# Kernel optimization log

Measured on AMD Instinct MI355X. Metric: run time of the kernel, lower is better.

## Reference

```python
import jax, jax.numpy as jnp
import numpy as np

N_SRC = 100000
N_DST = 50000
N_EDGES = 1600000
D_IN = 128
D_OUT = 64


def setup_inputs() -> dict:
    key = jax.random.key(0)
    ks = jax.random.split(key, 6)
    x = jax.random.normal(ks[0], (N_SRC, D_IN), dtype=jnp.float32)
    W_l = jax.random.normal(ks[1], (D_IN, D_OUT), dtype=jnp.float32) * (1.0 / np.sqrt(D_IN))
    b_l = jax.random.normal(ks[2], (D_OUT,), dtype=jnp.float32) * 0.01
    W_r = jax.random.normal(ks[3], (D_IN, D_OUT), dtype=jnp.float32) * (1.0 / np.sqrt(D_IN))
    src = jax.random.randint(ks[4], (N_EDGES,), 0, N_SRC, dtype=jnp.int64)
    dst = jax.random.randint(ks[5], (N_EDGES,), 0, N_DST, dtype=jnp.int64)
    edge_index = jnp.stack([src, dst], axis=0)
    return {"x": x, "W_l": W_l, "b_l": b_l, "W_r": W_r,
            "edge_index": edge_index, "n_dst": N_DST}


def reference(x, W_l, b_l, W_r, edge_index, n_dst):
    src, dst = edge_index[0], edge_index[1]
    # gather source features along edges: [E, D_in]
    msgs = x[src]
    # mean aggregation at destination nodes
    agg = jax.ops.segment_sum(msgs, dst, num_segments=n_dst)          # [n_dst, D_in]
    cnt = jax.ops.segment_sum(jnp.ones_like(dst, dtype=x.dtype), dst,
                              num_segments=n_dst)                     # [n_dst]
    mean = agg / jnp.maximum(cnt, 1.0)[:, None]
    x_target = x[:n_dst]
    # SAGEConv: lin_l(mean_agg) + lin_r(x_target)
    out = mean @ W_l + b_l + x_target @ W_r                           # [n_dst, D_out]
    return jax.nn.log_softmax(out, axis=-1)
```

## Files before the change

### kernel.cpp

```cpp
#include <hip/hip_runtime.h>
#include <math.h>

#define DIN  128
#define DOUT 64
#define PROWS 64
#define KS   32
#define XSP  36
#define BSH  6
#define BMSK 63
#define BCAP 2496

__device__ inline unsigned short f2bf(float f) {
    unsigned u = __float_as_uint(f);
    u += 0x7fffu + ((u >> 16) & 1u);
    return (unsigned short)(u >> 16);
}
__device__ inline float bflo(unsigned u) { return __uint_as_float(u << 16); }
__device__ inline float bfhi(unsigned u) { return __uint_as_float(u & 0xffff0000u); }

__global__ void __launch_bounds__(256) build_k(
    const int* __restrict__ ei, unsigned* __restrict__ gTail,
    int* __restrict__ bucketBuf,
    const float* __restrict__ x, const float* __restrict__ Wl,
    const float* __restrict__ bl, const float* __restrict__ Wr,
    unsigned short* __restrict__ y, float* __restrict__ zout,
    int E, int nFill, int P, int nyb, int n_src, int n_dst, int nB)
{
    __shared__ float s_mem[PROWS * XSP + KS * DOUT];
    const int b = blockIdx.x;
    const int fq = b / P;
    const bool isFill = ((b % P) == 0) && (fq < nFill);

    if (isFill) {
        int* s_i  = (int*)s_mem;
        int* lcnt = s_i;
        int* lpos = s_i + 1024;
        int* s_gb = s_i + 2048;
        const int t = threadIdx.x;
        const int myb = (fq * 256 + t) * 8;
        const bool full = (myb + 8 <= E);
        const bool any  = (myb < E);
        int4 sa, sb4, da, db;
        if (full) {
            sa  = *(const int4*)(ei + myb);
            sb4 = *(const int4*)(ei + myb + 4);
            da  = *(const int4*)(ei + E + myb);
            db  = *(const int4*)(ei + E + myb + 4);
        }
        lcnt[t] = 0; lcnt[t + 256] = 0; lcnt[t + 512] = 0; lcnt[t + 768] = 0;
        lpos[t] = 0; lpos[t + 256] = 0; lpos[t + 512] = 0; lpos[t + 768] = 0;
        __syncthreads();
        if (full) {
            atomicAdd(&lcnt[da.x >> BSH], 1); atomicAdd(&lcnt[da.y >> BSH], 1);
            atomicAdd(&lcnt[da.z >> BSH], 1); atomicAdd(&lcnt[da.w >> BSH], 1);
            atomicAdd(&lcnt[db.x >> BSH], 1); atomicAdd(&lcnt[db.y >> BSH], 1);
            atomicAdd(&lcnt[db.z >> BSH], 1); atomicAdd(&lcnt[db.w >> BSH], 1);
        } else if (any) {
            for (int i = myb; i < E && i < myb + 8; ++i)
                atomicAdd(&lcnt[ei[E + i] >> BSH], 1);
        }
        __syncthreads();
        for (int bk = t; bk < nB; bk += 256)
            s_gb[bk] = (int)atomicAdd(&gTail[bk], (unsigned)lcnt[bk]);
        __syncthreads();
#define PLACE(S, D) { int bk = (D) >> BSH; int p = atomicAdd(&lpos[bk], 1);          \
                      unsigned pos = (unsigned)(s_gb[bk] + p);                        \
                      if (pos < BCAP) bucketBuf[(size_t)bk * BCAP + pos] =            \
                          ((S) << BSH) | ((D) & BMSK); }
        if (full) {
            PLACE(sa.x,  da.x) PLACE(sa.y,  da.y) PLACE(sa.z,  da.z) PLACE(sa.w,  da.w)
            PLACE(sb4.x, db.x) PLACE(sb4.y, db.y) PLACE(sb4.z, db.z) PLACE(sb4.w, db.w)
        } else if (any) {
            for (int i = myb; i < E && i < myb + 8; ++i) {
                int s = ei[i], d = ei[E + i];
                PLACE(s, d)
            }
        }
#undef PLACE
        return;
    }

    const int fillsBefore = (fq + 1 < nFill) ? (fq + 1) : nFill;
    const int pb = b - fillsBefore;
    const int t  = threadIdx.x;
    const bool isY = (pb < nyb);
    const int rowBase = (isY ? pb : pb - nyb) * PROWS;
    const int nRows = isY ? n_src : n_dst;
    const float* __restrict__ W = isY ? Wl : Wr;

    float* s_xs = s_mem;
    float* s_ws = s_mem + PROWS * XSP;

    const int cg = t & 15;
    const int rg = t >> 4;
    const int r0 = rg * 4;

    float4 acc0 = {0.f,0.f,0.f,0.f};
    float4 acc1 = {0.f,0.f,0.f,0.f};
    float4 acc2 = {0.f,0.f,0.f,0.f};
    float4 acc3 = {0.f,0.f,0.f,0.f};

#define ROWFMA(acc, xv)                                                                     \
    acc.x = fmaf(xv.w, w3.x, fmaf(xv.z, w2.x, fmaf(xv.y, w1.x, fmaf(xv.x, w0.x, acc.x)))); \
    acc.y = fmaf(xv.w, w3.y, fmaf(xv.z, w2.y, fmaf(xv.y, w1.y, fmaf(xv.x, w0.y, acc.y)))); \
    acc.z = fmaf(xv.w, w3.z, fmaf(xv.z, w2.z, fmaf(xv.y, w1.z, fmaf(xv.x, w0.z, acc.z)))); \
    acc.w = fmaf(xv.w, w3.w, fmaf(xv.z, w2.w, fmaf(xv.y, w1.w, fmaf(xv.x, w0.w, acc.w))));

    for (int k0 = 0; k0 < DIN; k0 += KS) {
        {
            const float* xs = x + (size_t)rowBase * DIN + k0;
            #pragma unroll
            for (int j = 0; j < 2; ++j) {
                int fi = t + 256 * j;
                int row = fi >> 3, c4 = fi & 7;
                if (rowBase + row < nRows) {
                    float4 v = *(const float4*)(xs + (size_t)row * DIN + c4 * 4);
                    *(float4*)(&s_xs[row * XSP + c4 * 4]) = v;
                }
            }
            const float* ws = W + (size_t)k0 * DOUT;
            #pragma unroll
            for (int j = 0; j < 2; ++j) {
                int fi = t + 256 * j;
                int row = fi >> 4, c4 = fi & 15;
                float4 v = *(const float4*)(ws + row * DOUT + c4 * 4);
                *(float4*)(&s_ws[row * DOUT + c4 * 4]) = v;
            }
        }
        __syncthreads();

        const float* wp = s_ws + cg * 4;
        #pragma unroll 2
        for (int k = 0; k < KS; k += 4) {
            float4 w0 = *(const float4*)(wp + (k + 0) * DOUT);
            float4 w1 = *(const float4*)(wp + (k + 1) * DOUT);
            float4 w2 = *(const float4*)(wp + (k + 2) * DOUT);
            float4 w3 = *(const float4*)(wp + (k + 3) * DOUT);
            float4 x0 = *(const float4*)(&s_xs[(r0 + 0) * XSP + k]);
            float4 x1 = *(const float4*)(&s_xs[(r0 + 1) * XSP + k]);
            float4 x2 = *(const float4*)(&s_xs[(r0 + 2) * XSP + k]);
            float4 x3 = *(const float4*)(&s_xs[(r0 + 3) * XSP + k]);
            ROWFMA(acc0, x0)
            ROWFMA(acc1, x1)
            ROWFMA(acc2, x2)
            ROWFMA(acc3, x3)
        }
        __syncthreads();
    }
#undef ROWFMA

    if (isY) {
        float4 av[4] = {acc0, acc1, acc2, acc3};
        #pragma unroll
        for (int r = 0; r < 4; ++r) {
            int row = rowBase + r0 + r;
            if (row < nRows) {
                uint2 pk;
                pk.x = (unsigned)f2bf(av[r].x) | ((unsigned)f2bf(av[r].y) << 16);
                pk.y = (unsigned)f2bf(av[r].z) | ((unsigned)f2bf(av[r].w) << 16);
                *(uint2*)(y + (size_t)row * DOUT + cg * 4) = pk;
            }
        }
    } else {
        const float4 bv = *(const float4*)(bl + cg * 4);
        float4 av[4] = {acc0, acc1, acc2, acc3};
        #pragma unroll
        for (int r = 0; r < 4; ++r) {
            int row = rowBase + r0 + r;
            if (row < nRows) {
                float4 o;
                o.x = av[r].x + bv.x; o.y = av[r].y + bv.y;
                o.z = av[r].z + bv.z; o.w = av[r].w + bv.w;
                *(float4*)(zout + (size_t)row * DOUT + cg * 4) = o;
            }
        }
    }
}

__global__ void __launch_bounds__(512) bg_k(
    const unsigned* __restrict__ gTail, const int* __restrict__ bucketBuf,
    const unsigned short* __restrict__ y,
    float* __restrict__ out, int n_dst)
{
    __shared__ int s_ent[BCAP];
    __shared__ int s_csr[BCAP];
    __shared__ int s_hist[64];
    __shared__ int s_ofs[64];
    __shared__ int s_start[65];
    const int b = blockIdx.x, t = threadIdx.x;
    const int lane = t & 63, wave = t >> 6;

    if (t < 64) s_hist[t] = 0;
    int m = (int)gTail[b]; if (m > BCAP) m = BCAP;
    __syncthreads();

    const int* bb = bucketBuf + (size_t)b * BCAP;
    const int4* bb4 = (const int4*)bb;
    int4* se4 = (int4*)s_ent;
    const int m4 = m >> 2;
    for (int i4 = t; i4 < m4; i4 += 512) {
        int4 e4 = bb4[i4];
        se4[i4] = e4;
        atomicAdd(&s_hist[e4.x & BMSK], 1);
        atomicAdd(&s_hist[e4.y & BMSK], 1);
        atomicAdd(&s_hist[e4.z & BMSK], 1);
        atomicAdd(&s_hist[e4.w & BMSK], 1);
    }
    for (int i = (m4 << 2) + t; i < m; i += 512) {
        int e = bb[i];
        s_ent[i] = e;
        atomicAdd(&s_hist[e & BMSK], 1);
    }
    __syncthreads();

    if (wave == 0) {
        int h = s_hist[lane];
        int v = h;
        for (int o = 1; o < 64; o <<= 1) {
            int u = __shfl_up(v, o);
            if (lane >= o) v += u;
        }
        s_start[lane + 1] = v;
        if (lane == 0) s_start[0] = 0;
        s_ofs[lane] = v - h;
    }
    __syncthreads();

    for (int i4 = t; i4 < m4; i4 += 512) {
        int4 e4 = se4[i4];
        int p0 = atomicAdd(&s_ofs[e4.x & BMSK], 1); s_csr[p0] = e4.x >> BSH;
        int p1 = atomicAdd(&s_ofs[e4.y & BMSK], 1); s_csr[p1] = e4.y >> BSH;
        int p2 = atomicAdd(&s_ofs[e4.z & BMSK], 1); s_csr[p2] = e4.z >> BSH;
        int p3 = atomicAdd(&s_ofs[e4.w & BMSK], 1); s_csr[p3] = e4.w >> BSH;
    }
    for (int i = (m4 << 2) + t; i < m; i += 512) {
        int e = s_ent[i];
        int p = atomicAdd(&s_ofs[e & BMSK], 1);
        s_csr[p] = e >> BSH;
    }
    __syncthreads();

    const int dbase = b << BSH;
    int nloc = n_dst - dbase; if (nloc > 64) nloc = 64;
    const int g  = lane >> 3;
    const int c8 = lane & 7;
    const uint4* yw = (const uint4*)y;

#define ACC8(al, ah, u)                                              \
    al.x += bflo(u.x); al.y += bfhi(u.x);                            \
    al.z += bflo(u.y); al.w += bfhi(u.y);                            \
    ah.x += bflo(u.z); ah.y += bfhi(u.z);                            \
    ah.z += bflo(u.w); ah.w += bfhi(u.w);

    for (int r = wave; r < nloc; r += 8) {
        const int row = dbase + r;
        const int start = s_start[r];
        const int deg = s_start[r + 1] - start;

        const float4 zv0 = *(const float4*)(out + (size_t)row * DOUT + c8 * 8);
        const float4 zv1 = *(const float4*)(out + (size_t)row * DOUT + c8 * 8 + 4);

        float4 a0l = {0,0,0,0}, a0h = {0,0,0,0};
        float4 a1l = {0,0,0,0}, a1h = {0,0,0,0};
        float4 a2l = {0,0,0,0}, a2h = {0,0,0,0};
        float4 a3l = {0,0,0,0}, a3h = {0,0,0,0};

        for (int co = 0; co < deg; co += 64) {
            int rem = deg - co; if (rem > 64) rem = 64;
            int idx = (lane < rem) ? s_csr[start + co + lane] : 0;
            int i = 0;
            for (; i + 32 <= rem; i += 32) {
                int s0 = __shfl(idx, i + g);
                int s1 = __shfl(idx, i + 8 + g);
                int s2 = __shfl(idx, i + 16 + g);
                int s3 = __shfl(idx, i + 24 + g);
                uint4 u0 = yw[(size_t)s0 * 8 + c8];
                uint4 u1 = yw[(size_t)s1 * 8 + c8];
                uint4 u2 = yw[(size_t)s2 * 8 + c8];
                uint4 u3 = yw[(size_t)s3 * 8 + c8];
                ACC8(a0l, a0h, u0)
                ACC8(a1l, a1h, u1)
                ACC8(a2l, a2h, u2)
                ACC8(a3l, a3h, u3)
            }
            for (; i < rem; i += 8) {
                int e = i + g;
                int s0 = __shfl(idx, e);
                if (e < rem) {
                    uint4 u = yw[(size_t)s0 * 8 + c8];
                    ACC8(a0l, a0h, u)
                }
            }
        }

        float4 sl, sh;
        sl.x = (a0l.x + a1l.x) + (a2l.x + a3l.x);
        sl.y = (a0l.y + a1l.y) + (a2l.y + a3l.y);
        sl.z = (a0l.z + a1l.z) + (a2l.z + a3l.z);
        sl.w = (a0l.w + a1l.w) + (a2l.w + a3l.w);
        sh.x = (a0h.x + a1h.x) + (a2h.x + a3h.x);
        sh.y = (a0h.y + a1h.y) + (a2h.y + a3h.y);
        sh.z = (a0h.z + a1h.z) + (a2h.z + a3h.z);
        sh.w = (a0h.w + a1h.w) + (a2h.w + a3h.w);

        #pragma unroll
        for (int o = 32; o >= 8; o >>= 1) {
            sl.x += __shfl_xor(sl.x, o); sl.y += __shfl_xor(sl.y, o);
            sl.z += __shfl_xor(sl.z, o); sl.w += __shfl_xor(sl.w, o);
            sh.x += __shfl_xor(sh.x, o); sh.y += __shfl_xor(sh.y, o);
            sh.z += __shfl_xor(sh.z, o); sh.w += __shfl_xor(sh.w, o);
        }

        const float scale = 1.0f / (float)(deg > 0 ? deg : 1);
        float4 v0, v1;
        v0.x = sl.x * scale + zv0.x; v0.y = sl.y * scale + zv0.y;
        v0.z = sl.z * scale + zv0.z; v0.w = sl.w * scale + zv0.w;
        v1.x = sh.x * scale + zv1.x; v1.y = sh.y * scale + zv1.y;
        v1.z = sh.z * scale + zv1.z; v1.w = sh.w * scale + zv1.w;

        float mx = fmaxf(fmaxf(fmaxf(v0.x, v0.y), fmaxf(v0.z, v0.w)),
                         fmaxf(fmaxf(v1.x, v1.y), fmaxf(v1.z, v1.w)));
        for (int o = 4; o >= 1; o >>= 1) mx = fmaxf(mx, __shfl_xor(mx, o));
        float s = expf(v0.x - mx) + expf(v0.y - mx) + expf(v0.z - mx) + expf(v0.w - mx)
                + expf(v1.x - mx) + expf(v1.y - mx) + expf(v1.z - mx) + expf(v1.w - mx);
        for (int o = 4; o >= 1; o >>= 1) s += __shfl_xor(s, o);
        const float lse = mx + logf(s);

        if (lane < 8) {
            float4 o0, o1;
            o0.x = v0.x - lse; o0.y = v0.y - lse; o0.z = v0.z - lse; o0.w = v0.w - lse;
            o1.x = v1.x - lse; o1.y = v1.y - lse; o1.z = v1.z - lse; o1.w = v1.w - lse;
            *(float4*)(out + (size_t)row * DOUT + c8 * 8)     = o0;
            *(float4*)(out + (size_t)row * DOUT + c8 * 8 + 4) = o1;
        }
    }
#undef ACC8
}

extern "C" void kernel_launch(void* const* d_in, const int* in_sizes, int n_in,
                              void* d_out, int out_size, void* d_ws, size_t ws_size,
                              hipStream_t stream)
{
    const float* x  = (const float*)d_in[0];
    const float* Wl = (const float*)d_in[1];
    const float* bl = (const float*)d_in[2];
    const float* Wr = (const float*)d_in[3];
    const int*   ei = (const int*)d_in[4];

    const int E     = in_sizes[4] / 2;
    const int n_src = in_sizes[0] / DIN;
    const int n_dst = out_size / DOUT;
    const int nB    = (n_dst + (1 << BSH) - 1) >> BSH;

    unsigned* gTail = (unsigned*)d_ws;
    int* bucketBuf = (int*)d_ws + 1024;
    unsigned short* yb = (unsigned short*)(bucketBuf + (size_t)nB * BCAP);

    hipMemsetAsync(gTail, 0, 1024 * sizeof(unsigned), stream);

    int nFill = (E + 2047) / 2048;
    int nyb = (n_src + PROWS - 1) / PROWS;
    int nzb = (n_dst + PROWS - 1) / PROWS;
    int total = nFill + nyb + nzb;
    int P = (total + nFill - 1) / nFill;

    build_k<<<total, 256, 0, stream>>>(
        ei, gTail, bucketBuf, x, Wl, bl, Wr, yb, (float*)d_out,
        E, nFill, P, nyb, n_src, n_dst, nB);

    bg_k<<<nB, 512, 0, stream>>>(gTail, bucketBuf, yb, (float*)d_out, n_dst);
}
```

Before: 200.5 us.

## Use direct global-to-LDS loads with XOR swizzle and pad bucket tail counters

The projection tiles now load straight into LDS through the global_load_lds builtin instead of staging through registers. The padded x tile is replaced by an XOR-swizzled layout so the reads stay free of bank conflicts. Bucket tail counters are spread GSTR words apart to cut atomic contention and false sharing across cache lines, which makes the memset larger. The direct LDS load has alignment and layout rules on AMD hardware, and tail rows with no loaded data now leave stale LDS contents.

Result: slower. 215.1 us (+7.3%).

```diff
diff --git a/kernel.cpp b/kernel.cpp
--- a/kernel.cpp
+++ b/kernel.cpp
@@ -5,10 +5,10 @@
 #define DOUT 64
 #define PROWS 64
 #define KS   32
-#define XSP  36
 #define BSH  6
 #define BMSK 63
 #define BCAP 2496
+#define GSTR 16
 
 __device__ inline unsigned short f2bf(float f) {
     unsigned u = __float_as_uint(f);
@@ -17,6 +17,12 @@
 }
 __device__ inline float bflo(unsigned u) { return __uint_as_float(u << 16); }
 __device__ inline float bfhi(unsigned u) { return __uint_as_float(u & 0xffff0000u); }
+
+__device__ inline void gl16(const float* g, float* l) {
+    __builtin_amdgcn_global_load_lds(
+        (const __attribute__((address_space(1))) unsigned int*)g,
+        (__attribute__((address_space(3))) unsigned int*)l, 16, 0, 0);
+}
 
 __global__ void __launch_bounds__(256) build_k(
     const int* __restrict__ ei, unsigned* __restrict__ gTail,
@@ -26,7 +32,7 @@
     unsigned short* __restrict__ y, float* __restrict__ zout,
     int E, int nFill, int P, int nyb, int n_src, int n_dst, int nB)
 {
-    __shared__ float s_mem[PROWS * XSP + KS * DOUT];
+    __shared__ float s_mem[4096];
     const int b = blockIdx.x;
     const int fq = b / P;
     const bool isFill = ((b % P) == 0) && (fq < nFill);
@@ -61,7 +67,7 @@
         }
         __syncthreads();
         for (int bk = t; bk < nB; bk += 256)
-            s_gb[bk] = (int)atomicAdd(&gTail[bk], (unsigned)lcnt[bk]);
+            s_gb[bk] = (int)atomicAdd(&gTail[(size_t)bk * GSTR], (unsigned)lcnt[bk]);
         __syncthreads();
 #define PLACE(S, D) { int bk = (D) >> BSH; int p = atomicAdd(&lpos[bk], 1);          \
                       unsigned pos = (unsigned)(s_gb[bk] + p);                        \
@@ -89,11 +95,21 @@
     const float* __restrict__ W = isY ? Wl : Wr;
 
     float* s_xs = s_mem;
-    float* s_ws = s_mem + PROWS * XSP;
+    float* s_ws = s_mem + 2048;
 
     const int cg = t & 15;
     const int rg = t >> 4;
     const int r0 = rg * 4;
+
+    const int xrow0 = t >> 3,        xc0 = t & 7;
+    const int xrow1 = (t + 256) >> 3, xc1 = (t + 256) & 7;
+    const int xs0 = (xc0 ^ (xrow0 & 7)) * 4;
+    const int xs1 = (xc1 ^ (xrow1 & 7)) * 4;
+
+    const int xb0 = (r0 + 0) * 32, xm0 = (r0 + 0) & 7;
+    const int xb1 = (r0 + 1) * 32, xm1 = (r0 + 1) & 7;
+    const int xb2 = (r0 + 2) * 32, xm2 = (r0 + 2) & 7;
+    const int xb3 = (r0 + 3) * 32, xm3 = (r0 + 3) & 7;
 
     float4 acc0 = {0.f,0.f,0.f,0.f};
     float4 acc1 = {0.f,0.f,0.f,0.f};
@@ -109,37 +125,28 @@
     for (int k0 = 0; k0 < DIN; k0 += KS) {
         {
             const float* xs = x + (size_t)rowBase * DIN + k0;
-            #pragma unroll
-            for (int j = 0; j < 2; ++j) {
-                int fi = t + 256 * j;
-                int row = fi >> 3, c4 = fi & 7;
-                if (rowBase + row < nRows) {
-                    float4 v = *(const float4*)(xs + (size_t)row * DIN + c4 * 4);
-                    *(float4*)(&s_xs[row * XSP + c4 * 4]) = v;
-                }
-            }
+            if (rowBase + xrow0 < nRows)
+                gl16(xs + (size_t)xrow0 * DIN + xs0, s_xs + t * 4);
+            if (rowBase + xrow1 < nRows)
+                gl16(xs + (size_t)xrow1 * DIN + xs1, s_xs + (t + 256) * 4);
             const float* ws = W + (size_t)k0 * DOUT;
-            #pragma unroll
-            for (int j = 0; j < 2; ++j) {
-                int fi = t + 256 * j;
-                int row = fi >> 4, c4 = fi & 15;
-                float4 v = *(const float4*)(ws + row * DOUT + c4 * 4);
-                *(float4*)(&s_ws[row * DOUT + c4 * 4]) = v;
-            }
+            gl16(ws + t * 4,         s_ws + t * 4);
+            gl16(ws + (t + 256) * 4, s_ws + (t + 256) * 4);
         }
         __syncthreads();
 
         const float* wp = s_ws + cg * 4;
         #pragma unroll 2
         for (int k = 0; k < KS; k += 4) {
+            const int k4 = k >> 2;
             float4 w0 = *(const float4*)(wp + (k + 0) * DOUT);
             float4 w1 = *(const float4*)(wp + (k + 1) * DOUT);
             float4 w2 = *(const float4*)(wp + (k + 2) * DOUT);
             float4 w3 = *(const float4*)(wp + (k + 3) * DOUT);
-            float4 x0 = *(const float4*)(&s_xs[(r0 + 0) * XSP + k]);
-            float4 x1 = *(const float4*)(&s_xs[(r0 + 1) * XSP + k]);
-            float4 x2 = *(const float4*)(&s_xs[(r0 + 2) * XSP + k]);
-            float4 x3 = *(const float4*)(&s_xs[(r0 + 3) * XSP + k]);
+            float4 x0 = *(const float4*)(&s_xs[xb0 + ((k4 ^ xm0) << 2)]);
+            float4 x1 = *(const float4*)(&s_xs[xb1 + ((k4 ^ xm1) << 2)]);
+            float4 x2 = *(const float4*)(&s_xs[xb2 + ((k4 ^ xm2) << 2)]);
+            float4 x3 = *(const float4*)(&s_xs[xb3 + ((k4 ^ xm3) << 2)]);
             ROWFMA(acc0, x0)
             ROWFMA(acc1, x1)
             ROWFMA(acc2, x2)
@@ -191,7 +198,7 @@
     const int lane = t & 63, wave = t >> 6;
 
     if (t < 64) s_hist[t] = 0;
-    int m = (int)gTail[b]; if (m > BCAP) m = BCAP;
+    int m = (int)gTail[(size_t)b * GSTR]; if (m > BCAP) m = BCAP;
     __syncthreads();
 
     const int* bb = bucketBuf + (size_t)b * BCAP;
@@ -353,10 +360,10 @@
     const int nB    = (n_dst + (1 << BSH) - 1) >> BSH;
 
     unsigned* gTail = (unsigned*)d_ws;
-    int* bucketBuf = (int*)d_ws + 1024;
+    int* bucketBuf = (int*)d_ws + (size_t)nB * GSTR;
     unsigned short* yb = (unsigned short*)(bucketBuf + (size_t)nB * BCAP);
 
-    hipMemsetAsync(gTail, 0, 1024 * sizeof(unsigned), stream);
+    hipMemsetAsync(gTail, 0, (size_t)nB * GSTR * sizeof(unsigned), stream);
 
     int nFill = (E + 2047) / 2048;
     int nyb = (n_src + PROWS - 1) / PROWS;
```
